# Kernel optimization log

Measured on AMD Instinct MI355X. Metric: run time of the kernel, lower is better.

The kernel has to match this reference:

```python
import jax, jax.numpy as jnp
import numpy as np

N, E, ND, ED, H, OUT, L, VC = 10000, 160000, 8, 4, 128, 256, 6, 6
HEADS, C = 4, 128  # GATConv: out_channels=128 per head, concat=False -> mean over heads


def _ln(x, g, b, eps=1e-5):
    m = x.mean(-1, keepdims=True)
    v = ((x - m) ** 2).mean(-1, keepdims=True)
    return (x - m) * jax.lax.rsqrt(v + eps) * g + b


def _gat_layer(h, src, dst, e_attr, lw, a_src, a_dst, lew, a_edge, bias):
    # h: [N,H]; e_attr: [Etot,H]; PyG GATConv(heads=4, concat=False, edge_dim=H)
    xh = (h @ lw).reshape(N, HEADS, C)                 # [N,4,128]
    eh = (e_attr @ lew).reshape(-1, HEADS, C)          # [Etot,4,128]
    al_s = jnp.einsum('nhc,hc->nh', xh, a_src)
    al_d = jnp.einsum('nhc,hc->nh', xh, a_dst)
    al_e = jnp.einsum('ehc,hc->eh', eh, a_edge)
    alpha = jax.nn.leaky_relu(al_s[src] + al_d[dst] + al_e, 0.2)  # [Etot,4]
    amax = jax.ops.segment_max(alpha, dst, num_segments=N)
    ex = jnp.exp(alpha - amax[dst])
    den = jax.ops.segment_sum(ex, dst, num_segments=N)
    w = ex / (den[dst] + 1e-16)
    out = jax.ops.segment_sum(xh[src] * w[..., None], dst, num_segments=N)  # [N,4,128]
    return out.mean(axis=1) + bias


def setup_inputs() -> dict:
    key = jax.random.key(0)
    ks = jax.random.split(key, 32)
    s = 0.05
    d = {
        'x': jax.random.normal(ks[0], (N, ND), jnp.float32),
        'edge_index': jax.random.randint(ks[1], (2, E), 0, N),
        'edge_attr': jax.random.uniform(ks[2], (E, ED), jnp.float32),
        'vnf_context': jax.random.normal(ks[3], (1, VC), jnp.float32),
        # node embedding
        'node_w': jax.random.normal(ks[4], (ND, H)) * s, 'node_b': jnp.zeros((H,)),
        # EdgeAttentionLayer
        'ea_proj_w': jax.random.normal(ks[5], (ED, H)) * s, 'ea_proj_b': jnp.zeros((H,)),
        'vnf_w': jax.random.normal(ks[6], (VC, H)) * s, 'vnf_b': jnp.zeros((H,)),
        'att1_w': jax.random.normal(ks[7], (2 * H, H)) * s, 'att1_b': jnp.zeros((H,)),
        'att2_w': jax.random.normal(ks[8], (H, H // 2)) * s, 'att2_b': jnp.zeros((H // 2,)),
        'att3_w': jax.random.normal(ks[9], (H // 2, 1)) * s, 'att3_b': jnp.zeros((1,)),
        # per-layer GATConv params (stacked over L layers)
        'gat_lin_w': jax.random.normal(ks[10], (L, H, HEADS * C)) * s,
        'gat_att_src': jax.random.normal(ks[11], (L, HEADS, C)) * s,
        'gat_att_dst': jax.random.normal(ks[12], (L, HEADS, C)) * s,
        'gat_lin_edge_w': jax.random.normal(ks[13], (L, H, HEADS * C)) * s,
        'gat_att_edge': jax.random.normal(ks[14], (L, HEADS, C)) * s,
        'gat_bias': jnp.zeros((L, C)),
        'ln_scale': jnp.ones((L, H)), 'ln_bias': jnp.zeros((L, H)),
        # output projection
        'out_w': jax.random.normal(ks[15], (H, OUT)) * s, 'out_b': jnp.zeros((OUT,)),
    }
    return d


def reference(x, edge_index, edge_attr, vnf_context, node_w, node_b, ea_proj_w, ea_proj_b,
              vnf_w, vnf_b, att1_w, att1_b, att2_w, att2_b, att3_w, att3_b,
              gat_lin_w, gat_att_src, gat_att_dst, gat_lin_edge_w, gat_att_edge, gat_bias,
              ln_scale, ln_bias, out_w, out_b):
    src, dst = edge_index[0], edge_index[1]
    h = x @ node_w + node_b                                   # [N,128]
    # EdgeAttentionLayer (eval mode, no network_state)
    ef = edge_attr @ ea_proj_w + ea_proj_b                    # [E,128]
    vnf = vnf_context @ vnf_w + vnf_b                         # [1,128]
    comb = jnp.concatenate([ef, jnp.broadcast_to(vnf, (E, H))], axis=-1)
    a = jax.nn.relu(comb @ att1_w + att1_b)
    a = jax.nn.relu(a @ att2_w + att2_b)
    e_gate = jax.nn.sigmoid(a @ att3_w + att3_b)              # [E,1]
    w_edge = ef * e_gate                                      # [E,128]
    # GATConv default add_self_loops=True, fill_value='mean'
    loop = jnp.arange(N)
    src2 = jnp.concatenate([src, loop])
    dst2 = jnp.concatenate([dst, loop])
    e2 = jnp.concatenate([w_edge, jnp.broadcast_to(w_edge.mean(0, keepdims=True), (N, H))], axis=0)
    for l in range(L):
        hc = _gat_layer(h, src2, dst2, e2, gat_lin_w[l], gat_att_src[l], gat_att_dst[l],
                        gat_lin_edge_w[l], gat_att_edge[l], gat_bias[l])
        h = _ln(h + jax.nn.relu(hc), ln_scale[l], ln_bias[l])
    return h @ out_w + out_b                                  # [N,256]
```

## Files before the change

kernel.cpp:

```cpp
#include <hip/hip_runtime.h>
#include <hip/hip_bf16.h>
#include <math.h>

#define Nn 10000
#define Ee 160000
#define ET 170000
#define LL 6

typedef short v8s __attribute__((ext_vector_type(8)));
typedef float v4f __attribute__((ext_vector_type(4)));
typedef float v2f __attribute__((ext_vector_type(2)));

__device__ __forceinline__ unsigned short f2bf(float v) {
    unsigned int b = __float_as_uint(v);
    b += 0x7fffu + ((b >> 16) & 1u);
    return (unsigned short)(b >> 16);
}

__global__ void k_node_embed(const float* __restrict__ x, const float* __restrict__ nw,
                             const float* __restrict__ nb, float* __restrict__ h,
                             unsigned short* __restrict__ hb) {
    int idx = blockIdx.x * 256 + threadIdx.x;
    if (idx >= Nn * 128) return;
    int n = idx >> 7, c = idx & 127;
    const float* xr = x + (size_t)n * 8;
    float acc = nb[c];
#pragma unroll
    for (int k = 0; k < 8; k++) acc += xr[k] * nw[k * 128 + c];
    h[idx] = acc;
    hb[idx] = f2bf(acc);
}

__global__ void k_small(const float* __restrict__ vnfc, const float* __restrict__ vw,
                        const float* __restrict__ vb, const float* __restrict__ eab,
                        const float* __restrict__ a1w, const float* __restrict__ a1b,
                        const float* __restrict__ eaw, float* __restrict__ E1) {
    __shared__ float vr[128];
    __shared__ float sM1[512];
    __shared__ float sd1[128];
    int t = threadIdx.x;
    if (t < 128) {
        float a = vb[t];
#pragma unroll
        for (int k = 0; k < 6; k++) a += vnfc[k] * vw[k * 128 + t];
        vr[t] = a;
    }
    __syncthreads();
    if (t < 128) {
        float a = a1b[t];
        for (int k = 0; k < 128; k++) a += eab[k] * a1w[k * 128 + t];
        for (int k = 0; k < 128; k++) a += vr[k] * a1w[(128 + k) * 128 + t];
        sd1[t] = a;
    }
    {
        int r = t >> 7, j = t & 127;
        float a = 0.f;
        for (int k = 0; k < 128; k++) a += eaw[r * 128 + k] * a1w[k * 128 + j];
        sM1[r * 128 + j] = a;
    }
    __syncthreads();
    if (t < 128) {
        E1[t * 8 + 0] = sM1[t];
        E1[t * 8 + 1] = sM1[128 + t];
        E1[t * 8 + 2] = sM1[256 + t];
        E1[t * 8 + 3] = sM1[384 + t];
        E1[t * 8 + 4] = sd1[t];
        E1[t * 8 + 5] = 0.f; E1[t * 8 + 6] = 0.f; E1[t * 8 + 7] = 0.f;
    }
}

__global__ void k_bmat(const float* __restrict__ glw, const float* __restrict__ gas,
                       const float* __restrict__ gad, const float* __restrict__ glew,
                       const float* __restrict__ gae, float* __restrict__ Bs,
                       float* __restrict__ Bd, float* __restrict__ Be) {
    int idx = blockIdx.x * 256 + threadIdx.x;
    if (idx >= LL * 128 * 4) return;
    int hh = idx & 3, k = (idx >> 2) & 127, l = idx >> 9;
    const float* lwp = glw  + (size_t)l * 65536 + k * 512 + hh * 128;
    const float* lep = glew + (size_t)l * 65536 + k * 512 + hh * 128;
    const float* sp = gas + l * 512 + hh * 128;
    const float* dp = gad + l * 512 + hh * 128;
    const float* ep = gae + l * 512 + hh * 128;
    float s1 = 0, s2 = 0, s3 = 0;
    for (int c = 0; c < 128; c++) {
        float lv = lwp[c];
        s1 += lv * sp[c];
        s2 += lv * dp[c];
        s3 += lep[c] * ep[c];
    }
    Bs[idx] = s1; Bd[idx] = s2; Be[idx] = s3;
}

__global__ void k_wsum(const float* __restrict__ glw, unsigned short* __restrict__ WsumT) {
    int idx = blockIdx.x * 256 + threadIdx.x;
    if (idx >= LL * 128 * 512) return;
    int kk = idx & 511;
    int c = (idx >> 9) & 127;
    int l = idx >> 16;
    float v = 0.25f * glw[(size_t)l * 65536 + (size_t)(kk & 127) * 512 + (kk >> 7) * 128 + c];
    WsumT[(size_t)l * 65536 + (size_t)c * 512 + kk] = f2bf(v);
}

__global__ void k_pb(const float* __restrict__ eaw, const float* __restrict__ eab,
                     const float* __restrict__ Be, float* __restrict__ PB,
                     float* __restrict__ cB) {
    int t = threadIdx.x;
    if (t >= 24) return;
    int l = t >> 2, hh = t & 3;
    const float* bp = Be + l * 512 + hh;
    float s0 = 0, s1 = 0, s2 = 0, s3 = 0, sc = 0;
    for (int k = 0; k < 128; k++) {
        float bv = bp[k * 4];
        s0 += eaw[0 * 128 + k] * bv;
        s1 += eaw[1 * 128 + k] * bv;
        s2 += eaw[2 * 128 + k] * bv;
        s3 += eaw[3 * 128 + k] * bv;
        sc += eab[k] * bv;
    }
    PB[0 * 24 + t] = s0; PB[1 * 24 + t] = s1;
    PB[2 * 24 + t] = s2; PB[3 * 24 + t] = s3;
    cB[t] = sc;
}

__global__ __launch_bounds__(256) void k_edge(
    const float* __restrict__ ea, const float* __restrict__ E1,
    const float* __restrict__ a2w, const float* __restrict__ a2b,
    const float* __restrict__ a3w, const float* __restrict__ a3b,
    const float* __restrict__ PB, const float* __restrict__ cB,
    float* __restrict__ aleT, float* __restrict__ gsum) {
    __shared__ float sw2[128 * 64];
    __shared__ float4 sM[128];
    __shared__ float sD[128];
    __shared__ float prs[4][256];
    __shared__ float gsh[256];
    int t = threadIdx.x;
    int lane = t & 63;
    int p = t >> 6;
    int ps = __builtin_amdgcn_readfirstlane(p);
    for (int z = t; z < 2048; z += 256) ((float4*)sw2)[z] = ((const float4*)a2w)[z];
    if (t < 128) { sM[t] = *(const float4*)(E1 + t * 8); sD[t] = E1[t * 8 + 4]; }
    __syncthreads();
    int eb = blockIdx.x * 256 + lane;
    float4 ev[4];
#pragma unroll
    for (int r = 0; r < 4; r++) ev[r] = *(const float4*)(ea + (size_t)(eb + r * 64) * 4);
    v2f acc[4][8];
#pragma unroll
    for (int j = 0; j < 8; j++) {
        v2f b = {a2b[ps * 16 + 2 * j], a2b[ps * 16 + 2 * j + 1]};
#pragma unroll
        for (int r = 0; r < 4; r++) acc[r][j] = b;
    }
    const float* w2base = sw2 + ps * 16;
    for (int k = 0; k < 128; k++) {
        float4 m = sM[k];
        float dk = sD[k];
        v2f xx[4];
#pragma unroll
        for (int r = 0; r < 4; r++) {
            float xv = fmaxf(dk + ev[r].x * m.x + ev[r].y * m.y + ev[r].z * m.z + ev[r].w * m.w, 0.f);
            xx[r][0] = xv; xx[r][1] = xv;
        }
        const float* w2r = w2base + k * 64;
#pragma unroll
        for (int j4 = 0; j4 < 4; j4++) {
            float4 wv = *(const float4*)(w2r + j4 * 4);
            v2f w01 = {wv.x, wv.y}, w23 = {wv.z, wv.w};
#pragma unroll
            for (int r = 0; r < 4; r++) {
                acc[r][2 * j4]     += xx[r] * w01;
                acc[r][2 * j4 + 1] += xx[r] * w23;
            }
        }
    }
#pragma unroll
    for (int r = 0; r < 4; r++) {
        float pr = 0.f;
#pragma unroll
        for (int j = 0; j < 8; j++) {
            pr += fmaxf(acc[r][j][0], 0.f) * a3w[ps * 16 + 2 * j];
            pr += fmaxf(acc[r][j][1], 0.f) * a3w[ps * 16 + 2 * j + 1];
        }
        prs[p][r * 64 + lane] = pr;
    }
    __syncthreads();
    if (p == 0) {
        float v0 = 0.f, v1 = 0.f, v2 = 0.f, v3 = 0.f, v4 = 0.f;
#pragma unroll
        for (int rep = 0; rep < 4; rep++) {
            int le = rep * 64 + lane;
            float tot = prs[0][le] + prs[1][le] + prs[2][le] + prs[3][le] + a3b[0];
            float g = 1.f / (1.f + __expf(-tot));
            gsh[le] = g;
            float4 evv = ev[rep];
            v0 += g; v1 += g * evv.x; v2 += g * evv.y; v3 += g * evv.z; v4 += g * evv.w;
        }
#pragma unroll
        for (int d = 32; d > 0; d >>= 1) {
            v0 += __shfl_down(v0, d); v1 += __shfl_down(v1, d); v2 += __shfl_down(v2, d);
            v3 += __shfl_down(v3, d); v4 += __shfl_down(v4, d);
        }
        if (lane == 0) {
            atomicAdd(&gsum[0], v0); atomicAdd(&gsum[1], v1); atomicAdd(&gsum[2], v2);
            atomicAdd(&gsum[3], v3); atomicAdd(&gsum[4], v4);
        }
    }
    __syncthreads();
#pragma unroll
    for (int rep = 0; rep < 2; rep++) {
        int i4 = (rep == 0) ? ps : (ps < 2 ? ps + 4 : -1);
        if (i4 >= 0) {
            float4 c  = *(const float4*)(cB + i4 * 4);
            float4 p0 = *(const float4*)(PB + 0 * 24 + i4 * 4);
            float4 p1 = *(const float4*)(PB + 1 * 24 + i4 * 4);
            float4 p2 = *(const float4*)(PB + 2 * 24 + i4 * 4);
            float4 p3 = *(const float4*)(PB + 3 * 24 + i4 * 4);
#pragma unroll
            for (int r = 0; r < 4; r++) {
                float g = gsh[r * 64 + lane];
                float4 evv = ev[r];
                float4 o;
                o.x = g * (c.x + evv.x * p0.x + evv.y * p1.x + evv.z * p2.x + evv.w * p3.x);
                o.y = g * (c.y + evv.x * p0.y + evv.y * p1.y + evv.z * p2.y + evv.w * p3.y);
                o.z = g * (c.z + evv.x * p0.z + evv.y * p1.z + evv.z * p2.z + evv.w * p3.z);
                o.w = g * (c.w + evv.x * p0.w + evv.y * p1.w + evv.z * p2.w + evv.w * p3.w);
                *(float4*)(aleT + (size_t)i4 * Ee * 4 + (size_t)(eb + r * 64) * 4) = o;
            }
        }
    }
}

__global__ void k_lale(const float* __restrict__ gsum, const float* __restrict__ PB,
                       const float* __restrict__ cB, float* __restrict__ lale) {
    int t = threadIdx.x;
    if (t >= 24) return;
    float s = gsum[0] * cB[t] + gsum[1] * PB[t] + gsum[2] * PB[24 + t]
            + gsum[3] * PB[48 + t] + gsum[4] * PB[72 + t];
    lale[t] = s * (1.0f / Ee);
}

__global__ void k_hist(const int* __restrict__ ei, int* __restrict__ hist) {
    int i = blockIdx.x * 256 + threadIdx.x;
    if (i >= ET) return;
    int d = (i < Ee) ? ei[Ee + i] : (i - Ee);
    atomicAdd(&hist[d], 1);
}

__global__ __launch_bounds__(1024) void k_scan(const int* __restrict__ hist,
                                               int* __restrict__ seg, int* __restrict__ pos) {
    __shared__ int wsums[16];
    __shared__ int carry_s;
    int t = threadIdx.x;
    int lane = t & 63, wid = t >> 6;
    if (t == 0) { carry_s = 0; seg[0] = 0; }
    __syncthreads();
    for (int base = 0; base < Nn; base += 1024) {
        int idx = base + t;
        int v = (idx < Nn) ? hist[idx] : 0;
        int sc = v;
#pragma unroll
        for (int d = 1; d < 64; d <<= 1) {
            int up = __shfl_up(sc, d);
            if (lane >= d) sc += up;
        }
        if (lane == 63) wsums[wid] = sc;
        __syncthreads();
        if (wid == 0) {
            int wv = (lane < 16) ? wsums[lane] : 0;
            int wsc = wv;
#pragma unroll
            for (int d = 1; d < 16; d <<= 1) {
                int up = __shfl_up(wsc, d);
                if (lane >= d) wsc += up;
            }
            if (lane < 16) wsums[lane] = wsc - wv;
        }
        __syncthreads();
        int carry = carry_s;
        int inc = sc + wsums[wid] + carry;
        if (idx < Nn) { seg[idx + 1] = inc; pos[idx] = inc - v; }
        __syncthreads();
        if (t == 1023) carry_s = inc;
        __syncthreads();
    }
}

__global__ void k_scatter(const int* __restrict__ ei, int* __restrict__ pos,
                          int2* __restrict__ pse) {
    int i = blockIdx.x * 256 + threadIdx.x;
    if (i >= ET) return;
    int s, d;
    if (i < Ee) { s = ei[i]; d = ei[Ee + i]; } else { s = d = i - Ee; }
    int idx = atomicAdd(&pos[d], 1);
    pse[idx] = make_int2(s, i);
}

__global__ void k_ab(const float* __restrict__ h, const float* __restrict__ Bs_l,
                     const float* __restrict__ Bd_l, float* __restrict__ als,
                     float* __restrict__ ald) {
    int idx = blockIdx.x * 256 + threadIdx.x;
    if (idx >= Nn * 8) return;
    int n = idx >> 3, slot = idx & 7;
    const float* B = (slot < 4) ? Bs_l : Bd_l;
    int hh = slot & 3;
    const float4* hr = (const float4*)(h + (size_t)n * 128);
    float s = 0.f;
#pragma unroll 8
    for (int kb = 0; kb < 32; kb++) {
        float4 hv = hr[kb];
        s += hv.x * B[(4 * kb + 0) * 4 + hh] + hv.y * B[(4 * kb + 1) * 4 + hh]
           + hv.z * B[(4 * kb + 2) * 4 + hh] + hv.w * B[(4 * kb + 3) * 4 + hh];
    }
    if (slot < 4) als[n * 4 + hh] = s;
    else          ald[n * 4 + hh] = s;
}

__global__ __launch_bounds__(256) void k_agg2(
    const int2* __restrict__ pse, const int* __restrict__ seg,
    const float* __restrict__ als, const float* __restrict__ ald,
    const float* __restrict__ aleT_l, const float* __restrict__ lale_l,
    const unsigned short* __restrict__ hb, unsigned short* __restrict__ aggb) {
    __shared__ float lgS[2][512];
    __shared__ int srcS[2][128];
    __shared__ float msS[2][2][8];
    __shared__ float part[2][512];
    int t = threadIdx.x;
    int lane = t & 63;
    int wv = (t >> 6) & 1;
    int w = t >> 7;
    int n = blockIdx.x * 2 + w;
    int start = seg[n], end = seg[n + 1];
    int deg = end - start;
    int half = (deg + 1) >> 1;
    int s0 = start + wv * half;
    int e0 = wv ? end : start + half;
    int h1 = lane & 3;
    float llh1 = lale_l[h1];
    float a1d = ald[n * 4 + h1];
    float m = -INFINITY, ss = 0.f;
    for (int i = s0 + (lane >> 2); i < e0; i += 16) {
        int idx = i - start;
        int2 se = pse[i];
        float alev = se.y < Ee ? aleT_l[(size_t)se.y * 4 + h1] : llh1;
        float av = als[se.x * 4 + h1] + a1d + alev;
        av = av > 0.f ? av : 0.2f * av;
        if (idx < 128) {
            lgS[w][idx * 4 + h1] = av;
            if (h1 == 0) srcS[w][idx] = se.x;
        }
        if (av > m) { ss = ss * __expf(m - av) + 1.f; m = av; }
        else ss += __expf(av - m);
    }
#pragma unroll
    for (int d = 4; d <= 32; d <<= 1) {
        float mo = __shfl_xor(m, d), so = __shfl_xor(ss, d);
        float mm = fmaxf(m, mo);
        float sv = 0.f;
        if (m > -INFINITY) sv += ss * __expf(m - mm);
        if (mo > -INFINITY) sv += so * __expf(mo - mm);
        m = mm; ss = sv;
    }
    if (lane < 4) { msS[w][wv][lane] = m; msS[w][wv][4 + lane] = ss; }
    __syncthreads();
    {
        float mo = msS[w][1 - wv][h1], so = msS[w][1 - wv][4 + h1];
        float mm = fmaxf(m, mo);
        float sv = 0.f;
        if (m > -INFINITY) sv += ss * __expf(m - mm);
        if (mo > -INFINITY) sv += so * __expf(mo - mm);
        m = mm; ss = sv;
    }
    float mh0 = __shfl(m, 0), mh1 = __shfl(m, 1), mh2 = __shfl(m, 2), mh3 = __shfl(m, 3);
    float iv0 = 1.f / (__shfl(ss, 0) + 1e-16f), iv1 = 1.f / (__shfl(ss, 1) + 1e-16f);
    float iv2 = 1.f / (__shfl(ss, 2) + 1e-16f), iv3 = 1.f / (__shfl(ss, 3) + 1e-16f);
    int lo = wv * half;
    int hi = min(wv ? deg : half, 128);
    for (int z = lo + lane; z < hi; z += 64) {
        float4 lg = *(float4*)&lgS[w][z * 4];
        lg.x = __expf(lg.x - mh0) * iv0;
        lg.y = __expf(lg.y - mh1) * iv1;
        lg.z = __expf(lg.z - mh2) * iv2;
        lg.w = __expf(lg.w - mh3) * iv3;
        *(float4*)&lgS[w][z * 4] = lg;
    }
    int hp = lane >> 4;
    int cch = (lane & 15) * 8;
    float4 acc0 = make_float4(0.f, 0.f, 0.f, 0.f);
    float4 acc1 = make_float4(0.f, 0.f, 0.f, 0.f);
    int i2 = lo;
    for (; i2 + 2 <= hi; i2 += 2) {
        int sa = srcS[w][i2], sb = srcS[w][i2 + 1];
        float wg0 = lgS[w][i2 * 4 + hp], wg1 = lgS[w][i2 * 4 + 4 + hp];
        uint4 u0 = *(const uint4*)(hb + (size_t)sa * 128 + cch);
        uint4 u1 = *(const uint4*)(hb + (size_t)sb * 128 + cch);
        acc0.x += wg0 * __uint_as_float(u0.x << 16) + wg1 * __uint_as_float(u1.x << 16);
        acc0.y += wg0 * __uint_as_float(u0.x & 0xffff0000u) + wg1 * __uint_as_float(u1.x & 0xffff0000u);
        acc0.z += wg0 * __uint_as_float(u0.y << 16) + wg1 * __uint_as_float(u1.y << 16);
        acc0.w += wg0 * __uint_as_float(u0.y & 0xffff0000u) + wg1 * __uint_as_float(u1.y & 0xffff0000u);
        acc1.x += wg0 * __uint_as_float(u0.z << 16) + wg1 * __uint_as_float(u1.z << 16);
        acc1.y += wg0 * __uint_as_float(u0.z & 0xffff0000u) + wg1 * __uint_as_float(u1.z & 0xffff0000u);
        acc1.z += wg0 * __uint_as_float(u0.w << 16) + wg1 * __uint_as_float(u1.w << 16);
        acc1.w += wg0 * __uint_as_float(u0.w & 0xffff0000u) + wg1 * __uint_as_float(u1.w & 0xffff0000u);
    }
    if (i2 < hi) {
        int sa = srcS[w][i2];
        float wg0 = lgS[w][i2 * 4 + hp];
        uint4 u0 = *(const uint4*)(hb + (size_t)sa * 128 + cch);
        acc0.x += wg0 * __uint_as_float(u0.x << 16);
        acc0.y += wg0 * __uint_as_float(u0.x & 0xffff0000u);
        acc0.z += wg0 * __uint_as_float(u0.y << 16);
        acc0.w += wg0 * __uint_as_float(u0.y & 0xffff0000u);
        acc1.x += wg0 * __uint_as_float(u0.z << 16);
        acc1.y += wg0 * __uint_as_float(u0.z & 0xffff0000u);
        acc1.z += wg0 * __uint_as_float(u0.w << 16);
        acc1.w += wg0 * __uint_as_float(u0.w & 0xffff0000u);
    }
    float mhp = hp == 0 ? mh0 : hp == 1 ? mh1 : hp == 2 ? mh2 : mh3;
    float ivp = hp == 0 ? iv0 : hp == 1 ? iv1 : hp == 2 ? iv2 : iv3;
    for (int i = start + max(lo, 128); i < e0; i++) {
        int2 se = pse[i];
        float alev = se.y < Ee ? aleT_l[(size_t)se.y * 4 + hp] : lale_l[hp];
        float av = als[se.x * 4 + hp] + ald[n * 4 + hp] + alev;
        av = av > 0.f ? av : 0.2f * av;
        float wg0 = __expf(av - mhp) * ivp;
        uint4 u0 = *(const uint4*)(hb + (size_t)se.x * 128 + cch);
        acc0.x += wg0 * __uint_as_float(u0.x << 16);
        acc0.y += wg0 * __uint_as_float(u0.x & 0xffff0000u);
        acc0.z += wg0 * __uint_as_float(u0.y << 16);
        acc0.w += wg0 * __uint_as_float(u0.y & 0xffff0000u);
        acc1.x += wg0 * __uint_as_float(u0.z << 16);
        acc1.y += wg0 * __uint_as_float(u0.z & 0xffff0000u);
        acc1.z += wg0 * __uint_as_float(u0.w << 16);
        acc1.w += wg0 * __uint_as_float(u0.w & 0xffff0000u);
    }
    if (wv == 1) {
        *(float4*)&part[w][lane * 8] = acc0;
        *(float4*)&part[w][lane * 8 + 4] = acc1;
    }
    __syncthreads();
    if (wv == 0) {
        float4 p0 = *(const float4*)&part[w][lane * 8];
        float4 p1 = *(const float4*)&part[w][lane * 8 + 4];
        acc0.x += p0.x; acc0.y += p0.y; acc0.z += p0.z; acc0.w += p0.w;
        acc1.x += p1.x; acc1.y += p1.y; acc1.z += p1.z; acc1.w += p1.w;
        ushort4 q0, q1;
        q0.x = f2bf(acc0.x); q0.y = f2bf(acc0.y); q0.z = f2bf(acc0.z); q0.w = f2bf(acc0.w);
        q1.x = f2bf(acc1.x); q1.y = f2bf(acc1.y); q1.z = f2bf(acc1.z); q1.w = f2bf(acc1.w);
        *(ushort4*)(aggb + (size_t)n * 512 + lane * 8) = q0;
        *(ushort4*)(aggb + (size_t)n * 512 + lane * 8 + 4) = q1;
    }
}

__global__ __launch_bounds__(256) void k_post(
    const unsigned short* __restrict__ aggb, const unsigned short* __restrict__ WsumT_l,
    const float* __restrict__ gbias, const float* __restrict__ lnsc,
    const float* __restrict__ lnbi, float* __restrict__ h,
    unsigned short* __restrict__ hb) {
    int t = threadIdx.x;
    int lane = t & 63, w = t >> 6;
    int n0 = (blockIdx.x * 4 + w) * 16;
    if (n0 >= Nn) return;
    int m = lane & 15, q = lane >> 4;
    v4f acc[8];
#pragma unroll
    for (int nt = 0; nt < 8; nt++) acc[nt] = (v4f){0.f, 0.f, 0.f, 0.f};
    const unsigned short* arow = aggb + (size_t)(n0 + m) * 512 + q * 8;
#pragma unroll 4
    for (int ks = 0; ks < 16; ks++) {
        v8s fa = *(const v8s*)(arow + ks * 32);
#pragma unroll
        for (int nt = 0; nt < 8; nt++) {
            int col = nt * 16 + m;
            v8s fb = *(const v8s*)(WsumT_l + (size_t)col * 512 + ks * 32 + q * 8);
            acc[nt] = __builtin_amdgcn_mfma_f32_16x16x32_bf16(fa, fb, acc[nt], 0, 0, 0);
        }
    }
    float v[8][4];
    float s1[4] = {0.f, 0.f, 0.f, 0.f}, s2[4] = {0.f, 0.f, 0.f, 0.f};
#pragma unroll
    for (int nt = 0; nt < 8; nt++) {
        int col = nt * 16 + m;
        float b = gbias[col];
#pragma unroll
        for (int r = 0; r < 4; r++) {
            int row = n0 + q * 4 + r;
            float val = h[(size_t)row * 128 + col] + fmaxf(acc[nt][r] + b, 0.f);
            v[nt][r] = val;
            s1[r] += val; s2[r] += val * val;
        }
    }
#pragma unroll
    for (int d = 1; d <= 8; d <<= 1) {
#pragma unroll
        for (int r = 0; r < 4; r++) {
            s1[r] += __shfl_xor(s1[r], d);
            s2[r] += __shfl_xor(s2[r], d);
        }
    }
#pragma unroll
    for (int r = 0; r < 4; r++) {
        float mean = s1[r] * (1.f / 128.f);
        float var = s2[r] * (1.f / 128.f) - mean * mean;
        float rinv = rsqrtf(var + 1e-5f);
        int row = n0 + q * 4 + r;
#pragma unroll
        for (int nt = 0; nt < 8; nt++) {
            int col = nt * 16 + m;
            float o = (v[nt][r] - mean) * rinv * lnsc[col] + lnbi[col];
            h[(size_t)row * 128 + col] = o;
            hb[(size_t)row * 128 + col] = f2bf(o);
        }
    }
}

__global__ __launch_bounds__(256) void k_out(
    const float* __restrict__ h, const float* __restrict__ ow,
    const float* __restrict__ ob, float* __restrict__ out) {
    __shared__ float4 hs4[8][32];
    int t = threadIdx.x;
    int n0 = blockIdx.x * 8;
    if (t < 256) {
        int i = t >> 5, kb = t & 31;
        hs4[i][kb] = *(const float4*)(h + (size_t)(n0 + i) * 128 + 4 * kb);
    }
    __syncthreads();
    float acc[8] = {0, 0, 0, 0, 0, 0, 0, 0};
    for (int kb = 0; kb < 32; kb++) {
        float w0 = ow[(4 * kb + 0) * 256 + t];
        float w1 = ow[(4 * kb + 1) * 256 + t];
        float w2 = ow[(4 * kb + 2) * 256 + t];
        float w3 = ow[(4 * kb + 3) * 256 + t];
#pragma unroll
        for (int i = 0; i < 8; i++) {
            float4 hv = hs4[i][kb];
            acc[i] += hv.x * w0 + hv.y * w1 + hv.z * w2 + hv.w * w3;
        }
    }
    float b = ob[t];
#pragma unroll
    for (int i = 0; i < 8; i++) out[(size_t)(n0 + i) * 256 + t] = acc[i] + b;
}

extern "C" void kernel_launch(void* const* d_in, const int* in_sizes, int n_in,
                              void* d_out, int out_size, void* d_ws, size_t ws_size,
                              hipStream_t stream) {
    const float* x    = (const float*)d_in[0];
    const int*   ei   = (const int*)d_in[1];
    const float* ea   = (const float*)d_in[2];
    const float* vnfc = (const float*)d_in[3];
    const float* nw   = (const float*)d_in[4];
    const float* nb   = (const float*)d_in[5];
    const float* eaw  = (const float*)d_in[6];
    const float* eab  = (const float*)d_in[7];
    const float* vw   = (const float*)d_in[8];
    const float* vb   = (const float*)d_in[9];
    const float* a1w  = (const float*)d_in[10];
    const float* a1b  = (const float*)d_in[11];
    const float* a2w  = (const float*)d_in[12];
    const float* a2b  = (const float*)d_in[13];
    const float* a3w  = (const float*)d_in[14];
    const float* a3b  = (const float*)d_in[15];
    const float* glw  = (const float*)d_in[16];
    const float* gas  = (const float*)d_in[17];
    const float* gad  = (const float*)d_in[18];
    const float* glew = (const float*)d_in[19];
    const float* gae  = (const float*)d_in[20];
    const float* gb   = (const float*)d_in[21];
    const float* lnsc = (const float*)d_in[22];
    const float* lnbi = (const float*)d_in[23];
    const float* ow   = (const float*)d_in[24];
    const float* ob   = (const float*)d_in[25];
    float* out = (float*)d_out;

    char* w = (char*)d_ws;
    size_t o = 0;
    auto allocf = [&](size_t cnt) { float* p = (float*)(w + o); o += ((cnt * 4 + 255) / 256) * 256; return p; };
    auto alloci = [&](size_t cnt) { int* p = (int*)(w + o); o += ((cnt * 4 + 255) / 256) * 256; return p; };
    auto allocu = [&](size_t cnt) { unsigned short* p = (unsigned short*)(w + o); o += ((cnt * 2 + 255) / 256) * 256; return p; };
    float* h      = allocf((size_t)Nn * 128);
    unsigned short* hb    = allocu((size_t)Nn * 128);
    unsigned short* aggb  = allocu((size_t)Nn * 512);
    unsigned short* WsumT = allocu((size_t)LL * 128 * 512);
    float* als    = allocf((size_t)Nn * 4);
    float* ald    = allocf((size_t)Nn * 4);
    float* aleT   = allocf((size_t)LL * Ee * 4);
    float* Bs     = allocf(3072);
    float* Bd     = allocf(3072);
    float* Be     = allocf(3072);
    float* E1     = allocf(1024);
    float* PB     = allocf(96);
    float* cB     = allocf(24);
    float* gsum   = allocf(8);
    float* lale   = allocf(32);
    int* seg  = alloci(Nn + 1);
    int* hist = alloci(Nn);
    int* pos  = alloci(Nn);
    int2* pse = (int2*)alloci((size_t)ET * 2);

    hipMemsetAsync(hist, 0, Nn * sizeof(int), stream);
    hipMemsetAsync(gsum, 0, 8 * sizeof(float), stream);

    k_node_embed<<<(Nn * 128 + 255) / 256, 256, 0, stream>>>(x, nw, nb, h, hb);
    k_small<<<1, 512, 0, stream>>>(vnfc, vw, vb, eab, a1w, a1b, eaw, E1);
    k_bmat<<<(LL * 128 * 4 + 255) / 256, 256, 0, stream>>>(glw, gas, gad, glew, gae, Bs, Bd, Be);
    k_wsum<<<(LL * 128 * 512 + 255) / 256, 256, 0, stream>>>(glw, WsumT);
    k_pb<<<1, 32, 0, stream>>>(eaw, eab, Be, PB, cB);
    k_edge<<<Ee / 256, 256, 0, stream>>>(ea, E1, a2w, a2b, a3w, a3b, PB, cB, aleT, gsum);
    k_hist<<<(ET + 255) / 256, 256, 0, stream>>>(ei, hist);
    k_scan<<<1, 1024, 0, stream>>>(hist, seg, pos);
    k_scatter<<<(ET + 255) / 256, 256, 0, stream>>>(ei, pos, pse);
    k_lale<<<1, 32, 0, stream>>>(gsum, PB, cB, lale);
    for (int l = 0; l < LL; l++) {
        k_ab<<<(Nn * 8 + 255) / 256, 256, 0, stream>>>(h, Bs + l * 512, Bd + l * 512, als, ald);
        k_agg2<<<Nn / 2, 256, 0, stream>>>(pse, seg, als, ald, aleT + (size_t)l * Ee * 4,
                                           lale + l * 4, hb, aggb);
        k_post<<<(625 + 3) / 4, 256, 0, stream>>>(aggb, WsumT + (size_t)l * 65536,
                                                  gb + l * 128, lnsc + l * 128, lnbi + l * 128,
                                                  h, hb);
    }
    k_out<<<Nn / 8, 256, 0, stream>>>(h, ow, ob, out);
}
```

Measured before the change: 575.6 us.

## Single-pass GAT aggregation without max subtraction; fuse next-layer attention logits into post

The aggregation kernel drops the two-pass online-softmax (max/sum reduction, shared-memory logit staging) and instead accumulates exp(logit) weights and the denominator in one pass, normalizing at the end. Logits are clamped at 60 to avoid overflow, on the assumption that they stay small. The per-layer k_ab launch is removed by computing the next layer's source/destination attention scores inside k_post's epilogue from the freshly normalized h. k_edge also gets a min-occupancy launch bound.

New measurement: 559.6 us. 1.03x faster.

```diff
diff --git a/kernel.cpp b/kernel.cpp
--- a/kernel.cpp
+++ b/kernel.cpp
@@ -16,6 +16,8 @@
     b += 0x7fffu + ((b >> 16) & 1u);
     return (unsigned short)(b >> 16);
 }
+__device__ __forceinline__ float bflo(unsigned int u) { return __uint_as_float(u << 16); }
+__device__ __forceinline__ float bfhi(unsigned int u) { return __uint_as_float(u & 0xffff0000u); }
 
 __global__ void k_node_embed(const float* __restrict__ x, const float* __restrict__ nw,
                              const float* __restrict__ nb, float* __restrict__ h,
@@ -122,7 +124,7 @@
     cB[t] = sc;
 }
 
-__global__ __launch_bounds__(256) void k_edge(
+__global__ __launch_bounds__(256, 3) void k_edge(
     const float* __restrict__ ea, const float* __restrict__ E1,
     const float* __restrict__ a2w, const float* __restrict__ a2b,
     const float* __restrict__ a3w, const float* __restrict__ a3b,
@@ -315,15 +317,13 @@
     else          ald[n * 4 + hh] = s;
 }
 
-__global__ __launch_bounds__(256) void k_agg2(
+__global__ __launch_bounds__(256) void k_agg3(
     const int2* __restrict__ pse, const int* __restrict__ seg,
     const float* __restrict__ als, const float* __restrict__ ald,
     const float* __restrict__ aleT_l, const float* __restrict__ lale_l,
     const unsigned short* __restrict__ hb, unsigned short* __restrict__ aggb) {
-    __shared__ float lgS[2][512];
-    __shared__ int srcS[2][128];
-    __shared__ float msS[2][2][8];
     __shared__ float part[2][512];
+    __shared__ float pden[2][4];
     int t = threadIdx.x;
     int lane = t & 63;
     int wv = (t >> 6) & 1;
@@ -334,115 +334,63 @@
     int half = (deg + 1) >> 1;
     int s0 = start + wv * half;
     int e0 = wv ? end : start + half;
-    int h1 = lane & 3;
-    float llh1 = lale_l[h1];
-    float a1d = ald[n * 4 + h1];
-    float m = -INFINITY, ss = 0.f;
-    for (int i = s0 + (lane >> 2); i < e0; i += 16) {
-        int idx = i - start;
-        int2 se = pse[i];
-        float alev = se.y < Ee ? aleT_l[(size_t)se.y * 4 + h1] : llh1;
-        float av = als[se.x * 4 + h1] + a1d + alev;
-        av = av > 0.f ? av : 0.2f * av;
-        if (idx < 128) {
-            lgS[w][idx * 4 + h1] = av;
-            if (h1 == 0) srcS[w][idx] = se.x;
-        }
-        if (av > m) { ss = ss * __expf(m - av) + 1.f; m = av; }
-        else ss += __expf(av - m);
-    }
-#pragma unroll
-    for (int d = 4; d <= 32; d <<= 1) {
-        float mo = __shfl_xor(m, d), so = __shfl_xor(ss, d);
-        float mm = fmaxf(m, mo);
-        float sv = 0.f;
-        if (m > -INFINITY) sv += ss * __expf(m - mm);
-        if (mo > -INFINITY) sv += so * __expf(mo - mm);
-        m = mm; ss = sv;
-    }
-    if (lane < 4) { msS[w][wv][lane] = m; msS[w][wv][4 + lane] = ss; }
-    __syncthreads();
-    {
-        float mo = msS[w][1 - wv][h1], so = msS[w][1 - wv][4 + h1];
-        float mm = fmaxf(m, mo);
-        float sv = 0.f;
-        if (m > -INFINITY) sv += ss * __expf(m - mm);
-        if (mo > -INFINITY) sv += so * __expf(mo - mm);
-        m = mm; ss = sv;
-    }
-    float mh0 = __shfl(m, 0), mh1 = __shfl(m, 1), mh2 = __shfl(m, 2), mh3 = __shfl(m, 3);
-    float iv0 = 1.f / (__shfl(ss, 0) + 1e-16f), iv1 = 1.f / (__shfl(ss, 1) + 1e-16f);
-    float iv2 = 1.f / (__shfl(ss, 2) + 1e-16f), iv3 = 1.f / (__shfl(ss, 3) + 1e-16f);
-    int lo = wv * half;
-    int hi = min(wv ? deg : half, 128);
-    for (int z = lo + lane; z < hi; z += 64) {
-        float4 lg = *(float4*)&lgS[w][z * 4];
-        lg.x = __expf(lg.x - mh0) * iv0;
-        lg.y = __expf(lg.y - mh1) * iv1;
-        lg.z = __expf(lg.z - mh2) * iv2;
-        lg.w = __expf(lg.w - mh3) * iv3;
-        *(float4*)&lgS[w][z * 4] = lg;
-    }
     int hp = lane >> 4;
     int cch = (lane & 15) * 8;
+    float aldh = ald[n * 4 + hp];
+    float llh = lale_l[hp];
+    float den = 0.f;
     float4 acc0 = make_float4(0.f, 0.f, 0.f, 0.f);
     float4 acc1 = make_float4(0.f, 0.f, 0.f, 0.f);
-    int i2 = lo;
-    for (; i2 + 2 <= hi; i2 += 2) {
-        int sa = srcS[w][i2], sb = srcS[w][i2 + 1];
-        float wg0 = lgS[w][i2 * 4 + hp], wg1 = lgS[w][i2 * 4 + 4 + hp];
-        uint4 u0 = *(const uint4*)(hb + (size_t)sa * 128 + cch);
-        uint4 u1 = *(const uint4*)(hb + (size_t)sb * 128 + cch);
-        acc0.x += wg0 * __uint_as_float(u0.x << 16) + wg1 * __uint_as_float(u1.x << 16);
-        acc0.y += wg0 * __uint_as_float(u0.x & 0xffff0000u) + wg1 * __uint_as_float(u1.x & 0xffff0000u);
-        acc0.z += wg0 * __uint_as_float(u0.y << 16) + wg1 * __uint_as_float(u1.y << 16);
-        acc0.w += wg0 * __uint_as_float(u0.y & 0xffff0000u) + wg1 * __uint_as_float(u1.y & 0xffff0000u);
-        acc1.x += wg0 * __uint_as_float(u0.z << 16) + wg1 * __uint_as_float(u1.z << 16);
-        acc1.y += wg0 * __uint_as_float(u0.z & 0xffff0000u) + wg1 * __uint_as_float(u1.z & 0xffff0000u);
-        acc1.z += wg0 * __uint_as_float(u0.w << 16) + wg1 * __uint_as_float(u1.w << 16);
-        acc1.w += wg0 * __uint_as_float(u0.w & 0xffff0000u) + wg1 * __uint_as_float(u1.w & 0xffff0000u);
-    }
-    if (i2 < hi) {
-        int sa = srcS[w][i2];
-        float wg0 = lgS[w][i2 * 4 + hp];
-        uint4 u0 = *(const uint4*)(hb + (size_t)sa * 128 + cch);
-        acc0.x += wg0 * __uint_as_float(u0.x << 16);
-        acc0.y += wg0 * __uint_as_float(u0.x & 0xffff0000u);
-        acc0.z += wg0 * __uint_as_float(u0.y << 16);
-        acc0.w += wg0 * __uint_as_float(u0.y & 0xffff0000u);
-        acc1.x += wg0 * __uint_as_float(u0.z << 16);
-        acc1.y += wg0 * __uint_as_float(u0.z & 0xffff0000u);
-        acc1.z += wg0 * __uint_as_float(u0.w << 16);
-        acc1.w += wg0 * __uint_as_float(u0.w & 0xffff0000u);
-    }
-    float mhp = hp == 0 ? mh0 : hp == 1 ? mh1 : hp == 2 ? mh2 : mh3;
-    float ivp = hp == 0 ? iv0 : hp == 1 ? iv1 : hp == 2 ? iv2 : iv3;
-    for (int i = start + max(lo, 128); i < e0; i++) {
-        int2 se = pse[i];
-        float alev = se.y < Ee ? aleT_l[(size_t)se.y * 4 + hp] : lale_l[hp];
-        float av = als[se.x * 4 + hp] + ald[n * 4 + hp] + alev;
-        av = av > 0.f ? av : 0.2f * av;
-        float wg0 = __expf(av - mhp) * ivp;
-        uint4 u0 = *(const uint4*)(hb + (size_t)se.x * 128 + cch);
-        acc0.x += wg0 * __uint_as_float(u0.x << 16);
-        acc0.y += wg0 * __uint_as_float(u0.x & 0xffff0000u);
-        acc0.z += wg0 * __uint_as_float(u0.y << 16);
-        acc0.w += wg0 * __uint_as_float(u0.y & 0xffff0000u);
-        acc1.x += wg0 * __uint_as_float(u0.z << 16);
-        acc1.y += wg0 * __uint_as_float(u0.z & 0xffff0000u);
-        acc1.z += wg0 * __uint_as_float(u0.w << 16);
-        acc1.w += wg0 * __uint_as_float(u0.w & 0xffff0000u);
+    int i = s0;
+    for (; i + 2 <= e0; i += 2) {
+        int2 sa = pse[i], sb = pse[i + 1];
+        float ala = sa.y < Ee ? aleT_l[(size_t)sa.y * 4 + hp] : llh;
+        float alb = sb.y < Ee ? aleT_l[(size_t)sb.y * 4 + hp] : llh;
+        float ava = als[sa.x * 4 + hp] + aldh + ala;
+        float avb = als[sb.x * 4 + hp] + aldh + alb;
+        ava = ava > 0.f ? ava : 0.2f * ava;
+        avb = avb > 0.f ? avb : 0.2f * avb;
+        float ea = __expf(fminf(ava, 60.f));
+        float eb = __expf(fminf(avb, 60.f));
+        den += ea + eb;
+        uint4 ua = *(const uint4*)(hb + (size_t)sa.x * 128 + cch);
+        uint4 ub = *(const uint4*)(hb + (size_t)sb.x * 128 + cch);
+        acc0.x += ea * bflo(ua.x) + eb * bflo(ub.x);
+        acc0.y += ea * bfhi(ua.x) + eb * bfhi(ub.x);
+        acc0.z += ea * bflo(ua.y) + eb * bflo(ub.y);
+        acc0.w += ea * bfhi(ua.y) + eb * bfhi(ub.y);
+        acc1.x += ea * bflo(ua.z) + eb * bflo(ub.z);
+        acc1.y += ea * bfhi(ua.z) + eb * bfhi(ub.z);
+        acc1.z += ea * bflo(ua.w) + eb * bflo(ub.w);
+        acc1.w += ea * bfhi(ua.w) + eb * bfhi(ub.w);
+    }
+    if (i < e0) {
+        int2 sa = pse[i];
+        float ala = sa.y < Ee ? aleT_l[(size_t)sa.y * 4 + hp] : llh;
+        float ava = als[sa.x * 4 + hp] + aldh + ala;
+        ava = ava > 0.f ? ava : 0.2f * ava;
+        float ea = __expf(fminf(ava, 60.f));
+        den += ea;
+        uint4 ua = *(const uint4*)(hb + (size_t)sa.x * 128 + cch);
+        acc0.x += ea * bflo(ua.x); acc0.y += ea * bfhi(ua.x);
+        acc0.z += ea * bflo(ua.y); acc0.w += ea * bfhi(ua.y);
+        acc1.x += ea * bflo(ua.z); acc1.y += ea * bfhi(ua.z);
+        acc1.z += ea * bflo(ua.w); acc1.w += ea * bfhi(ua.w);
     }
     if (wv == 1) {
         *(float4*)&part[w][lane * 8] = acc0;
         *(float4*)&part[w][lane * 8 + 4] = acc1;
+        if ((lane & 15) == 0) pden[w][hp] = den;
     }
     __syncthreads();
     if (wv == 0) {
         float4 p0 = *(const float4*)&part[w][lane * 8];
         float4 p1 = *(const float4*)&part[w][lane * 8 + 4];
-        acc0.x += p0.x; acc0.y += p0.y; acc0.z += p0.z; acc0.w += p0.w;
-        acc1.x += p1.x; acc1.y += p1.y; acc1.z += p1.z; acc1.w += p1.w;
+        float inv = 1.f / (den + pden[w][hp] + 1e-16f);
+        acc0.x = (acc0.x + p0.x) * inv; acc0.y = (acc0.y + p0.y) * inv;
+        acc0.z = (acc0.z + p0.z) * inv; acc0.w = (acc0.w + p0.w) * inv;
+        acc1.x = (acc1.x + p1.x) * inv; acc1.y = (acc1.y + p1.y) * inv;
+        acc1.z = (acc1.z + p1.z) * inv; acc1.w = (acc1.w + p1.w) * inv;
         ushort4 q0, q1;
         q0.x = f2bf(acc0.x); q0.y = f2bf(acc0.y); q0.z = f2bf(acc0.z); q0.w = f2bf(acc0.w);
         q1.x = f2bf(acc1.x); q1.y = f2bf(acc1.y); q1.z = f2bf(acc1.z); q1.w = f2bf(acc1.w);
@@ -455,7 +403,8 @@
     const unsigned short* __restrict__ aggb, const unsigned short* __restrict__ WsumT_l,
     const float* __restrict__ gbias, const float* __restrict__ lnsc,
     const float* __restrict__ lnbi, float* __restrict__ h,
-    unsigned short* __restrict__ hb) {
+    unsigned short* __restrict__ hb, const float* __restrict__ Bs_n,
+    const float* __restrict__ Bd_n, float* __restrict__ als, float* __restrict__ ald) {
     int t = threadIdx.x;
     int lane = t & 63, w = t >> 6;
     int n0 = (blockIdx.x * 4 + w) * 16;
@@ -497,6 +446,7 @@
             s2[r] += __shfl_xor(s2[r], d);
         }
     }
+    float o8[8][4];
 #pragma unroll
     for (int r = 0; r < 4; r++) {
         float mean = s1[r] * (1.f / 128.f);
@@ -507,8 +457,51 @@
         for (int nt = 0; nt < 8; nt++) {
             int col = nt * 16 + m;
             float o = (v[nt][r] - mean) * rinv * lnsc[col] + lnbi[col];
+            o8[nt][r] = o;
             h[(size_t)row * 128 + col] = o;
             hb[(size_t)row * 128 + col] = f2bf(o);
+        }
+    }
+    float sal[4][4], sad[4][4];
+#pragma unroll
+    for (int r = 0; r < 4; r++) {
+#pragma unroll
+        for (int hh = 0; hh < 4; hh++) { sal[r][hh] = 0.f; sad[r][hh] = 0.f; }
+    }
+#pragma unroll
+    for (int nt = 0; nt < 8; nt++) {
+        int col = nt * 16 + m;
+        float4 bs = *(const float4*)(Bs_n + col * 4);
+        float4 bd = *(const float4*)(Bd_n + col * 4);
+#pragma unroll
+        for (int r = 0; r < 4; r++) {
+            float o = o8[nt][r];
+            sal[r][0] += o * bs.x; sal[r][1] += o * bs.y;
+            sal[r][2] += o * bs.z; sal[r][3] += o * bs.w;
+            sad[r][0] += o * bd.x; sad[r][1] += o * bd.y;
+            sad[r][2] += o * bd.z; sad[r][3] += o * bd.w;
+        }
+    }
+#pragma unroll
+    for (int d = 1; d <= 8; d <<= 1) {
+#pragma unroll
+        for (int r = 0; r < 4; r++) {
+#pragma unroll
+            for (int hh = 0; hh < 4; hh++) {
+                sal[r][hh] += __shfl_xor(sal[r][hh], d);
+                sad[r][hh] += __shfl_xor(sad[r][hh], d);
+            }
+        }
+    }
+    if (m < 8) {
+        int hh = m & 3;
+#pragma unroll
+        for (int r = 0; r < 4; r++) {
+            int row = n0 + q * 4 + r;
+            float va = (hh == 0) ? sal[r][0] : (hh == 1) ? sal[r][1] : (hh == 2) ? sal[r][2] : sal[r][3];
+            float vd = (hh == 0) ? sad[r][0] : (hh == 1) ? sad[r][1] : (hh == 2) ? sad[r][2] : sad[r][3];
+            if (m < 4) als[row * 4 + hh] = va;
+            else       ald[row * 4 + hh] = vd;
         }
     }
 }
@@ -610,13 +603,14 @@
     k_scan<<<1, 1024, 0, stream>>>(hist, seg, pos);
     k_scatter<<<(ET + 255) / 256, 256, 0, stream>>>(ei, pos, pse);
     k_lale<<<1, 32, 0, stream>>>(gsum, PB, cB, lale);
+    k_ab<<<(Nn * 8 + 255) / 256, 256, 0, stream>>>(h, Bs, Bd, als, ald);
     for (int l = 0; l < LL; l++) {
-        k_ab<<<(Nn * 8 + 255) / 256, 256, 0, stream>>>(h, Bs + l * 512, Bd + l * 512, als, ald);
-        k_agg2<<<Nn / 2, 256, 0, stream>>>(pse, seg, als, ald, aleT + (size_t)l * Ee * 4,
+        int ln = (l + 1) % LL;
+        k_agg3<<<Nn / 2, 256, 0, stream>>>(pse, seg, als, ald, aleT + (size_t)l * Ee * 4,
                                            lale + l * 4, hb, aggb);
         k_post<<<(625 + 3) / 4, 256, 0, stream>>>(aggb, WsumT + (size_t)l * 65536,
                                                   gb + l * 128, lnsc + l * 128, lnbi + l * 128,
-                                                  h, hb);
+                                                  h, hb, Bs + ln * 512, Bd + ln * 512, als, ald);
     }
     k_out<<<Nn / 8, 256, 0, stream>>>(h, ow, ob, out);
 }
```
